# Kernel tuning notes

Measured on AMD Instinct MI355X. Metric: run time of the kernel, lower is better.

Reference implementation:

```python
import jax, jax.numpy as jnp
import numpy as np

B, N, M, F1, F2 = 8, 128, 256, 256, 256


def setup_inputs() -> dict:
    key = jax.random.key(0)
    k = jax.random.split(key, 6)
    s = 1.0 / np.sqrt(F1)
    return {
        "x": jax.random.normal(k[0], (B, N, F1), dtype=jnp.float32),
        "y": jax.random.normal(k[1], (B, M, F2), dtype=jnp.float32),
        "U_w": jax.random.normal(k[2], (F2, F1), dtype=jnp.float32) * s,
        "U_b": jax.random.normal(k[3], (F2,), dtype=jnp.float32) * s,
        "W_w": jax.random.normal(k[4], (1, F2), dtype=jnp.float32) * (1.0 / np.sqrt(F2)),
        "W_b": jax.random.normal(k[5], (1,), dtype=jnp.float32) * (1.0 / np.sqrt(F2)),
    }


def reference(x, y, U_w, U_b, W_w, W_b):
    # poolAttn path (default). dropout=0 -> identity.
    u = jnp.einsum('bnf,gf->bng', x, U_w) + U_b          # [B,N,F2]
    # broadcast bilinear: tanh(u[:,:,None,:] * y[:,None,:,:]) -> [B,N,M,F2]
    a = jnp.tanh(u[:, :, None, :] * y[:, None, :, :])
    alpha = jnp.einsum('bnmf,f->bnm', a, W_w[0]) + W_b[0]  # [B,N,M]
    # x attention: max over M, softmax over N
    xw = jax.nn.softmax(alpha.max(axis=2), axis=1)         # [B,N]
    x_pooled = jnp.einsum('bnf,bn->bf', x, xw)             # [B,F1]
    # y attention: max over N, softmax over M
    yw = jax.nn.softmax(alpha.max(axis=1), axis=1)         # [B,M]
    y_pooled = jnp.einsum('bm,bmf->bf', yw, y)             # [B,F2]
    return jnp.concatenate([x_pooled, y_pooled], axis=1)   # [B,F1+F2]
```

## Files before the change

### kernel.cpp

```cpp
#include <hip/hip_runtime.h>
#include <math.h>

#define B_ 8
#define N_ 128
#define M_ 256
#define F_ 256

#define LOG2E2 2.8853900817779268f

__global__ __launch_bounds__(256) void k1_lite(const float* __restrict__ x,
                                               const float* __restrict__ Uw,
                                               const float* __restrict__ Ub,
                                               float* __restrict__ u) {
  const int g  = threadIdx.x;
  const int r0 = blockIdx.x * 4;
  const float* __restrict__ uwr = Uw + (size_t)g * F_;
  const float* __restrict__ xr  = x + (size_t)r0 * F_;

  float a0 = 0.f, a1 = 0.f, a2 = 0.f, a3 = 0.f;
#pragma unroll 4
  for (int f = 0; f < F_; f += 4) {
    const float4 wv = *(const float4*)&uwr[f];
    const float4 x0 = *(const float4*)&xr[0 * F_ + f];
    const float4 x1 = *(const float4*)&xr[1 * F_ + f];
    const float4 x2 = *(const float4*)&xr[2 * F_ + f];
    const float4 x3 = *(const float4*)&xr[3 * F_ + f];
    a0 = fmaf(wv.x, x0.x, a0); a0 = fmaf(wv.y, x0.y, a0);
    a0 = fmaf(wv.z, x0.z, a0); a0 = fmaf(wv.w, x0.w, a0);
    a1 = fmaf(wv.x, x1.x, a1); a1 = fmaf(wv.y, x1.y, a1);
    a1 = fmaf(wv.z, x1.z, a1); a1 = fmaf(wv.w, x1.w, a1);
    a2 = fmaf(wv.x, x2.x, a2); a2 = fmaf(wv.y, x2.y, a2);
    a2 = fmaf(wv.z, x2.z, a2); a2 = fmaf(wv.w, x2.w, a2);
    a3 = fmaf(wv.x, x3.x, a3); a3 = fmaf(wv.y, x3.y, a3);
    a3 = fmaf(wv.z, x3.z, a3); a3 = fmaf(wv.w, x3.w, a3);
  }
  const float ubv = Ub[g];
  u[(size_t)(r0 + 0) * F_ + g] = (a0 + ubv) * LOG2E2;
  u[(size_t)(r0 + 1) * F_ + g] = (a1 + ubv) * LOG2E2;
  u[(size_t)(r0 + 2) * F_ + g] = (a2 + ubv) * LOG2E2;
  u[(size_t)(r0 + 3) * F_ + g] = (a3 + ubv) * LOG2E2;
}

__global__ void k2_alpha(const float* __restrict__ u,
                         const float* __restrict__ y,
                         const float* __restrict__ Ww,
                         float* __restrict__ rminp,
                         float* __restrict__ cminp) {
  __shared__ float us[8][F_];
  __shared__ float red[8][8][64];
  __shared__ float sm[8][64];

  const int tid  = threadIdx.x;
  const int mg   = blockIdx.x;
  const int ns   = blockIdx.y;
  const int b    = blockIdx.z;
  const int n0   = ns * 8;
  const int m0   = mg * 64;
  const int lane = tid & 63;
  const int w    = tid >> 6;
  const int fc   = __builtin_amdgcn_readfirstlane(w);

  {
    const int r = tid >> 6, c = (tid & 63) * 4;
    *(float4*)&us[r][c] =
        *(const float4*)&u[(size_t)(b * N_ + n0 + r) * F_ + c];
  }

  float4 yv[8];
  float4 wwv[8];
  {
    const float* yr = y + ((size_t)(b * M_ + m0 + lane)) * F_ + fc * 32;
    const float* wr = Ww + fc * 32;
#pragma unroll
    for (int j = 0; j < 8; ++j) {
      yv[j]  = *(const float4*)&yr[4 * j];
      wwv[j] = *(const float4*)&wr[4 * j];
    }
  }
  __syncthreads();

#define QUAD(nn, j, S0, S1)                                                              \
  do {                                                                                   \
    const float4 uv = *(const float4*)&us[nn][fc * 32 + 4 * (j)];                        \
    S0 = fmaf(wwv[j].x,                                                                  \
              __builtin_amdgcn_rcpf(__builtin_amdgcn_exp2f(uv.x * yv[j].x) + 1.f), S0);  \
    S1 = fmaf(wwv[j].y,                                                                  \
              __builtin_amdgcn_rcpf(__builtin_amdgcn_exp2f(uv.y * yv[j].y) + 1.f), S1);  \
    S0 = fmaf(wwv[j].z,                                                                  \
              __builtin_amdgcn_rcpf(__builtin_amdgcn_exp2f(uv.z * yv[j].z) + 1.f), S0);  \
    S1 = fmaf(wwv[j].w,                                                                  \
              __builtin_amdgcn_rcpf(__builtin_amdgcn_exp2f(uv.w * yv[j].w) + 1.f), S1);  \
  } while (0)

#define DO_N(nn, A)                                                                      \
  do {                                                                                   \
    float s0 = 0.f, s1 = 0.f;                                                            \
    QUAD(nn, 0, s0, s1); QUAD(nn, 1, s0, s1); QUAD(nn, 2, s0, s1); QUAD(nn, 3, s0, s1);  \
    QUAD(nn, 4, s0, s1); QUAD(nn, 5, s0, s1); QUAD(nn, 6, s0, s1); QUAD(nn, 7, s0, s1);  \
    A = s0 + s1;                                                                         \
  } while (0)

  float a0, a1, a2, a3, a4, a5, a6, a7;
  DO_N(0, a0); DO_N(1, a1); DO_N(2, a2); DO_N(3, a3);
  DO_N(4, a4); DO_N(5, a5); DO_N(6, a6); DO_N(7, a7);
#undef DO_N
#undef QUAD

  red[0][fc][lane] = a0; red[1][fc][lane] = a1;
  red[2][fc][lane] = a2; red[3][fc][lane] = a3;
  red[4][fc][lane] = a4; red[5][fc][lane] = a5;
  red[6][fc][lane] = a6; red[7][fc][lane] = a7;
  __syncthreads();

  float S = 0.f;
#pragma unroll
  for (int k = 0; k < 8; ++k) S += red[w][k][lane];

  float r = S;
#pragma unroll
  for (int s = 32; s; s >>= 1) r = fminf(r, __shfl_xor(r, s));
  if (lane == 0) rminp[((size_t)b * 4 + mg) * N_ + n0 + w] = r;

  sm[w][lane] = S;
  __syncthreads();
  if (w == 0) {
    float c = sm[0][lane];
#pragma unroll
    for (int k = 1; k < 8; ++k) c = fminf(c, sm[k][lane]);
    cminp[((size_t)b * 16 + ns) * M_ + m0 + lane] = c;
  }
}

__global__ __launch_bounds__(1024) void kb_final(
    const float* __restrict__ x, const float* __restrict__ y,
    const float* __restrict__ rminp, const float* __restrict__ cminp,
    float* __restrict__ out) {
  const int b = blockIdx.x;
  const int task = blockIdx.y;
  const int tid = threadIdx.x;
  const int wv = tid >> 6;
  __shared__ float wgt[M_];
  __shared__ float red[16];
  __shared__ float part[4][256];

  if (task == 0) {
    float rv = -INFINITY;
    if (tid < N_) {
      float v = INFINITY;
#pragma unroll
      for (int mg = 0; mg < 4; ++mg)
        v = fminf(v, rminp[((size_t)b * 4 + mg) * N_ + tid]);
      rv = -2.f * v;
    }
    float m1 = rv;
#pragma unroll
    for (int s = 32; s; s >>= 1) m1 = fmaxf(m1, __shfl_xor(m1, s));
    if ((tid & 63) == 0) red[wv] = m1;
    __syncthreads();
    m1 = red[0];
#pragma unroll
    for (int k = 1; k < 16; ++k) m1 = fmaxf(m1, red[k]);
    __syncthreads();
    const float e1 = (tid < N_) ? __expf(rv - m1) : 0.f;
    float s1 = e1;
#pragma unroll
    for (int s = 32; s; s >>= 1) s1 += __shfl_xor(s1, s);
    if ((tid & 63) == 0) red[wv] = s1;
    __syncthreads();
    s1 = 0.f;
#pragma unroll
    for (int k = 0; k < 16; ++k) s1 += red[k];
    if (tid < N_) wgt[tid] = e1 / s1;
    __syncthreads();

    const int q = tid >> 8, f = tid & 255;
    float accx = 0.f;
#pragma unroll 4
    for (int n = q; n < N_; n += 4)
      accx = fmaf(wgt[n], x[(size_t)(b * N_ + n) * F_ + f], accx);
    part[q][f] = accx;
    __syncthreads();
    if (tid < 256)
      out[b * (2 * F_) + f] = part[0][f] + part[1][f] + part[2][f] + part[3][f];
  } else {
    float cv = -INFINITY;
    if (tid < M_) {
      float c = INFINITY;
#pragma unroll
      for (int ns = 0; ns < 16; ++ns)
        c = fminf(c, cminp[((size_t)b * 16 + ns) * M_ + tid]);
      cv = -2.f * c;
    }
    float m2 = cv;
#pragma unroll
    for (int s = 32; s; s >>= 1) m2 = fmaxf(m2, __shfl_xor(m2, s));
    if ((tid & 63) == 0) red[wv] = m2;
    __syncthreads();
    m2 = red[0];
#pragma unroll
    for (int k = 1; k < 16; ++k) m2 = fmaxf(m2, red[k]);
    __syncthreads();
    const float e2 = (tid < M_) ? __expf(cv - m2) : 0.f;
    float s2 = e2;
#pragma unroll
    for (int s = 32; s; s >>= 1) s2 += __shfl_xor(s2, s);
    if ((tid & 63) == 0) red[wv] = s2;
    __syncthreads();
    s2 = 0.f;
#pragma unroll
    for (int k = 0; k < 16; ++k) s2 += red[k];
    if (tid < M_) wgt[tid] = e2 / s2;
    __syncthreads();

    const int q = tid >> 8, f = tid & 255;
    float accy = 0.f;
#pragma unroll 4
    for (int m = q; m < M_; m += 4)
      accy = fmaf(wgt[m], y[(size_t)(b * M_ + m) * F_ + f], accy);
    part[q][f] = accy;
    __syncthreads();
    if (tid < 256)
      out[b * (2 * F_) + F_ + f] =
          part[0][f] + part[1][f] + part[2][f] + part[3][f];
  }
}

extern "C" void kernel_launch(void* const* d_in, const int* in_sizes, int n_in,
                              void* d_out, int out_size, void* d_ws, size_t ws_size,
                              hipStream_t stream) {
  (void)in_sizes; (void)n_in; (void)out_size; (void)ws_size;
  const float* x  = (const float*)d_in[0];
  const float* y  = (const float*)d_in[1];
  const float* Uw = (const float*)d_in[2];
  const float* Ub = (const float*)d_in[3];
  const float* Ww = (const float*)d_in[4];

  float* u     = (float*)d_ws;
  float* rminp = u + B_ * N_ * F_;
  float* cminp = rminp + B_ * 4 * N_;
  float* outp  = (float*)d_out;

  k1_lite<<<dim3((B_ * N_) / 4), 256, 0, stream>>>(x, Uw, Ub, u);
  k2_alpha<<<dim3(4, 16, B_), 512, 0, stream>>>(u, y, Ww, rminp, cminp);
  kb_final<<<dim3(B_, 2), 1024, 0, stream>>>(x, y, rminp, cminp, outp);
}
```

Baseline: 35.71 us.

## Stage y tiles through LDS with coalesced loads and split final kernel over features

In the alpha kernel, y is now loaded cooperatively with coalesced float4 reads into a padded shared tile in two halves, and each wave copies its slice into registers. Before, each lane read a strided 128-byte chunk of its own row. The final pooling kernel moves from 16 blocks of 1024 threads to 64 blocks of 256 threads, each handling a quarter of the features, which gives more parallelism in the tail. The cost is extra barriers, about 33KB more LDS in the alpha kernel (which may reduce occupancy), and softmax weights recomputed redundantly in every feature block.

```diff
diff --git a/kernel.cpp b/kernel.cpp
--- a/kernel.cpp
+++ b/kernel.cpp
@@ -47,6 +47,7 @@
                          float* __restrict__ rminp,
                          float* __restrict__ cminp) {
   __shared__ float us[8][F_];
+  __shared__ float ys[64][132];
   __shared__ float red[8][8][64];
   __shared__ float sm[8][64];
 
@@ -65,17 +66,40 @@
     *(float4*)&us[r][c] =
         *(const float4*)&u[(size_t)(b * N_ + n0 + r) * F_ + c];
   }
-
-  float4 yv[8];
   float4 wwv[8];
   {
-    const float* yr = y + ((size_t)(b * M_ + m0 + lane)) * F_ + fc * 32;
     const float* wr = Ww + fc * 32;
 #pragma unroll
-    for (int j = 0; j < 8; ++j) {
-      yv[j]  = *(const float4*)&yr[4 * j];
-      wwv[j] = *(const float4*)&wr[4 * j];
-    }
+    for (int j = 0; j < 8; ++j) wwv[j] = *(const float4*)&wr[4 * j];
+  }
+
+  float4 yv[8];
+  const float* __restrict__ ybase = y + (size_t)(b * M_ + m0) * F_;
+#pragma unroll
+  for (int k = 0; k < 4; ++k) {
+    const int flat = tid + k * 512;
+    const int row = flat >> 5, col = (flat & 31) * 4;
+    *(float4*)&ys[row][col] = *(const float4*)&ybase[(size_t)row * F_ + col];
+  }
+  __syncthreads();
+  if (w < 4) {
+    const int base = fc * 32;
+#pragma unroll
+    for (int j = 0; j < 8; ++j) yv[j] = *(const float4*)&ys[lane][base + 4 * j];
+  }
+  __syncthreads();
+#pragma unroll
+  for (int k = 0; k < 4; ++k) {
+    const int flat = tid + k * 512;
+    const int row = flat >> 5, col = (flat & 31) * 4;
+    *(float4*)&ys[row][col] =
+        *(const float4*)&ybase[(size_t)row * F_ + 128 + col];
+  }
+  __syncthreads();
+  if (w >= 4) {
+    const int base = (fc - 4) * 32;
+#pragma unroll
+    for (int j = 0; j < 8; ++j) yv[j] = *(const float4*)&ys[lane][base + 4 * j];
   }
   __syncthreads();
 
@@ -131,17 +155,18 @@
   }
 }
 
-__global__ __launch_bounds__(1024) void kb_final(
+__global__ __launch_bounds__(256) void kb_final(
     const float* __restrict__ x, const float* __restrict__ y,
     const float* __restrict__ rminp, const float* __restrict__ cminp,
     float* __restrict__ out) {
-  const int b = blockIdx.x;
+  const int b    = blockIdx.x;
   const int task = blockIdx.y;
-  const int tid = threadIdx.x;
-  const int wv = tid >> 6;
+  const int fq   = blockIdx.z;
+  const int tid  = threadIdx.x;
+  const int w    = tid >> 6;
   __shared__ float wgt[M_];
-  __shared__ float red[16];
-  __shared__ float part[4][256];
+  __shared__ float redv[4];
+  __shared__ float part[4][64];
 
   if (task == 0) {
     float rv = -INFINITY;
@@ -155,36 +180,34 @@
     float m1 = rv;
 #pragma unroll
     for (int s = 32; s; s >>= 1) m1 = fmaxf(m1, __shfl_xor(m1, s));
-    if ((tid & 63) == 0) red[wv] = m1;
-    __syncthreads();
-    m1 = red[0];
-#pragma unroll
-    for (int k = 1; k < 16; ++k) m1 = fmaxf(m1, red[k]);
+    if ((tid & 63) == 0) redv[w] = m1;
+    __syncthreads();
+    m1 = fmaxf(fmaxf(redv[0], redv[1]), fmaxf(redv[2], redv[3]));
     __syncthreads();
     const float e1 = (tid < N_) ? __expf(rv - m1) : 0.f;
     float s1 = e1;
 #pragma unroll
     for (int s = 32; s; s >>= 1) s1 += __shfl_xor(s1, s);
-    if ((tid & 63) == 0) red[wv] = s1;
-    __syncthreads();
-    s1 = 0.f;
-#pragma unroll
-    for (int k = 0; k < 16; ++k) s1 += red[k];
+    if ((tid & 63) == 0) redv[w] = s1;
+    __syncthreads();
+    s1 = redv[0] + redv[1] + redv[2] + redv[3];
     if (tid < N_) wgt[tid] = e1 / s1;
     __syncthreads();
 
-    const int q = tid >> 8, f = tid & 255;
-    float accx = 0.f;
-#pragma unroll 4
+    const int f = fq * 64 + (tid & 63);
+    const int q = w;
+    float acc = 0.f;
+#pragma unroll 8
     for (int n = q; n < N_; n += 4)
-      accx = fmaf(wgt[n], x[(size_t)(b * N_ + n) * F_ + f], accx);
-    part[q][f] = accx;
-    __syncthreads();
-    if (tid < 256)
-      out[b * (2 * F_) + f] = part[0][f] + part[1][f] + part[2][f] + part[3][f];
+      acc = fmaf(wgt[n], x[(size_t)(b * N_ + n) * F_ + f], acc);
+    part[q][tid & 63] = acc;
+    __syncthreads();
+    if (tid < 64)
+      out[b * (2 * F_) + fq * 64 + tid] =
+          part[0][tid] + part[1][tid] + part[2][tid] + part[3][tid];
   } else {
-    float cv = -INFINITY;
-    if (tid < M_) {
+    float cv;
+    {
       float c = INFINITY;
 #pragma unroll
       for (int ns = 0; ns < 16; ++ns)
@@ -194,34 +217,31 @@
     float m2 = cv;
 #pragma unroll
     for (int s = 32; s; s >>= 1) m2 = fmaxf(m2, __shfl_xor(m2, s));
-    if ((tid & 63) == 0) red[wv] = m2;
-    __syncthreads();
-    m2 = red[0];
-#pragma unroll
-    for (int k = 1; k < 16; ++k) m2 = fmaxf(m2, red[k]);
-    __syncthreads();
-    const float e2 = (tid < M_) ? __expf(cv - m2) : 0.f;
+    if ((tid & 63) == 0) redv[w] = m2;
+    __syncthreads();
+    m2 = fmaxf(fmaxf(redv[0], redv[1]), fmaxf(redv[2], redv[3]));
+    __syncthreads();
+    const float e2 = __expf(cv - m2);
     float s2 = e2;
 #pragma unroll
     for (int s = 32; s; s >>= 1) s2 += __shfl_xor(s2, s);
-    if ((tid & 63) == 0) red[wv] = s2;
-    __syncthreads();
-    s2 = 0.f;
-#pragma unroll
-    for (int k = 0; k < 16; ++k) s2 += red[k];
-    if (tid < M_) wgt[tid] = e2 / s2;
-    __syncthreads();
-
-    const int q = tid >> 8, f = tid & 255;
-    float accy = 0.f;
-#pragma unroll 4
+    if ((tid & 63) == 0) redv[w] = s2;
+    __syncthreads();
+    s2 = redv[0] + redv[1] + redv[2] + redv[3];
+    wgt[tid] = e2 / s2;
+    __syncthreads();
+
+    const int f = fq * 64 + (tid & 63);
+    const int q = w;
+    float acc = 0.f;
+#pragma unroll 8
     for (int m = q; m < M_; m += 4)
-      accy = fmaf(wgt[m], y[(size_t)(b * M_ + m) * F_ + f], accy);
-    part[q][f] = accy;
-    __syncthreads();
-    if (tid < 256)
-      out[b * (2 * F_) + F_ + f] =
-          part[0][f] + part[1][f] + part[2][f] + part[3][f];
+      acc = fmaf(wgt[m], y[(size_t)(b * M_ + m) * F_ + f], acc);
+    part[q][tid & 63] = acc;
+    __syncthreads();
+    if (tid < 64)
+      out[b * (2 * F_) + F_ + fq * 64 + tid] =
+          part[0][tid] + part[1][tid] + part[2][tid] + part[3][tid];
   }
 }
 
@@ -242,5 +262,5 @@
 
   k1_lite<<<dim3((B_ * N_) / 4), 256, 0, stream>>>(x, Uw, Ub, u);
   k2_alpha<<<dim3(4, 16, B_), 512, 0, stream>>>(u, y, Ww, rminp, cminp);
-  kb_final<<<dim3(B_, 2), 1024, 0, stream>>>(x, y, rminp, cminp, outp);
-}
+  kb_final<<<dim3(B_, 2, 4), 256, 0, stream>>>(x, y, rminp, cminp, outp);
+}
```

After: 35.56 us. About the same (-0.4%).
